# Kernel optimization log

Hardware: AMD Instinct MI355X
Metric: run time of the kernel (lower is better)

The kernel has to match this reference:

```python
import jax, jax.numpy as jnp
import numpy as np


def _skew_relative(QE):
    # QE: [B, H, N, 2N-1] -> [B, H, N, N] relative-position skew (Music-Transformer style)
    B, H, N, L = QE.shape  # L == 2N - 1
    x = jnp.pad(QE, ((0, 0), (0, 0), (0, 0), (0, 1))).reshape(B, H, N * (L + 1))
    x = jnp.pad(x, ((0, 0), (0, 0), (0, N - 1))).reshape(B, H, N + 1, 2 * N - 1)
    return x[:, :, :N, -N:]


def setup_inputs() -> dict:
    key = jax.random.key(0)
    ks = jax.random.split(key, 8)
    B, N, D, H, dh = 8, 1024, 512, 8, 64
    W_SCALE = 0.02
    return {
        "x": jax.random.normal(ks[0], (B, N, D), jnp.float32),
        "phase": jax.random.uniform(ks[1], (B, H, N, 1), jnp.float32),
        "E_rel": jax.random.normal(ks[2], (2 * N - 1, dh), jnp.float32) * 0.05,
        "W_q": jax.random.normal(ks[3], (H * dh, D), jnp.float32) * W_SCALE,
        "W_k": jax.random.normal(ks[4], (H * dh, D), jnp.float32) * W_SCALE,
        "W_v": jax.random.normal(ks[5], (H * dh, D), jnp.float32) * W_SCALE,
        "W_o": jax.random.normal(ks[6], (D, H * dh), jnp.float32) * W_SCALE,
        "b_o": jnp.zeros((D,), jnp.float32),
    }


def reference(x, phase, E_rel, W_q, W_k, W_v, W_o, b_o):
    B, N, _ = x.shape
    H = phase.shape[1]
    dh = W_q.shape[0] // H
    scale = 1.0 / (dh ** 0.5)

    def heads(W):  # [B,N,H*dh] -> [B,H,N,dh]
        return (x @ W.T).reshape(B, N, H, dh).transpose(0, 2, 1, 3)

    Q, K, V = heads(W_q), heads(W_k), heads(W_v)
    attn = jnp.einsum('bhnd,bhmd->bhnm', Q, K)
    attn = attn + _skew_relative(jnp.einsum('bhnd,ld->bhnl', Q, E_rel))
    attn = jax.nn.softmax(attn * scale, axis=-1)
    out = jnp.einsum('bhnm,bhmd->bhnd', attn, V) * phase  # phase-modulated AV
    out = out.transpose(0, 2, 1, 3).reshape(B, N, H * dh)
    return out @ W_o.T + b_o  # dropout is identity in eval mode
```

## Files before the change

### kernel.cpp

```cpp
#include <hip/hip_runtime.h>


typedef __bf16 bf16x8 __attribute__((ext_vector_type(8)));
typedef __bf16 bf16x4 __attribute__((ext_vector_type(4)));
typedef float  f32x4  __attribute__((ext_vector_type(4)));
typedef float  f32x16 __attribute__((ext_vector_type(16)));

#if __has_builtin(__builtin_amdgcn_exp2f)
#define EXP2(x) __builtin_amdgcn_exp2f(x)
#else
#define EXP2(x) exp2f(x)
#endif

#define GLOAD_LDS16(g, l)                                                      \
    __builtin_amdgcn_global_load_lds(                                          \
        (const __attribute__((address_space(1))) unsigned int*)(g),            \
        (__attribute__((address_space(3))) unsigned int*)(l), 16, 0, 0)


__global__ __launch_bounds__(256) void cvt_all(const float* __restrict__ x,
                                               const float* __restrict__ E,
                                               const float* __restrict__ wq,
                                               const float* __restrict__ wk,
                                               const float* __restrict__ wv,
                                               const float* __restrict__ wo,
                                               __bf16* __restrict__ xb,
                                               __bf16* __restrict__ Ef,
                                               __bf16* __restrict__ wqkv,
                                               __bf16* __restrict__ wob) {
    int i = blockIdx.x * 256 + threadIdx.x;
    if (i >= 1081328 ? i < 1343472 : i < 1048576) {
        const float* s; __bf16* d; int off;
        if      (i < 1048576) { s = x;  d = xb;            off = i; }
        else if (i < 1146864) { s = wq; d = wqkv;          off = i - 1081328; }
        else if (i < 1212400) { s = wk; d = wqkv + 262144; off = i - 1146864; }
        else if (i < 1277936) { s = wv; d = wqkv + 524288; off = i - 1212400; }
        else                  { s = wo; d = wob;           off = i - 1277936; }
        float4 v = *(const float4*)(s + (size_t)off * 4);
        bf16x4 o;
        o[0] = (__bf16)v.x; o[1] = (__bf16)v.y; o[2] = (__bf16)v.z; o[3] = (__bf16)v.w;
        *(bf16x4*)(d + (size_t)off * 4) = o;
    } else if (i >= 1048576 && i < 1081328) {
        int off = i - 1048576;
        float4 v = *(const float4*)(E + (size_t)off * 4);
        int e0i = off * 4;
        int l = e0i >> 6, d0 = e0i & 63;
        int t32 = l >> 5, cq = l & 31, ks = d0 >> 4, hf = (d0 >> 3) & 1, j = d0 & 7;
        bf16x4 o;
        o[0] = (__bf16)v.x; o[1] = (__bf16)v.y; o[2] = (__bf16)v.z; o[3] = (__bf16)v.w;
        *(bf16x4*)(Ef + ((size_t)((t32 * 4 + ks) * 64) + hf * 32 + cq) * 8 + j) = o;
    }
}

__global__ __launch_bounds__(256) void gemm_qkv(const __bf16* __restrict__ X,
                                                const __bf16* __restrict__ W,
                                                __bf16* __restrict__ Qb,
                                                __bf16* __restrict__ Kf,
                                                __bf16* __restrict__ Vf) {
    __shared__ __bf16 Xs[128][64];
    __shared__ __bf16 Ws[128][64];
    const int tid = threadIdx.x;
    const int wave = tid >> 6, lane = tid & 63;
    const int col = lane & 15, quad = lane >> 4;
    const int m_base = blockIdx.x * 128;
    const int j_base = blockIdx.y * 128;
    const bool qk = (j_base < 1024);
    const int wm = (wave & 1) * 64;
    const int wn = (wave >> 1) * 64;
    const f32x4 fz = {0.f, 0.f, 0.f, 0.f};
    f32x4 acc[4][4];
#pragma unroll
    for (int i = 0; i < 4; ++i)
#pragma unroll
        for (int j = 0; j < 4; ++j) acc[i][j] = fz;

    for (int k0 = 0; k0 < 512; k0 += 64) {
#pragma unroll
        for (int p = 0; p < 4; ++p) {
            int s = tid + p * 256;
            int row = s >> 3, cc = (s & 7) * 8;
            GLOAD_LDS16(X + (size_t)(m_base + row) * 512 + k0 + cc, &Xs[0][0] + (size_t)s * 8);
            GLOAD_LDS16(W + (size_t)(j_base + row) * 512 + k0 + cc, &Ws[0][0] + (size_t)s * 8);
        }
        __syncthreads();
#pragma unroll
        for (int kk = 0; kk < 64; kk += 32) {
            bf16x8 xa[4], wb[4];
#pragma unroll
            for (int i = 0; i < 4; ++i) xa[i] = *(const bf16x8*)(&Xs[wm + i * 16 + col][kk + quad * 8]);
#pragma unroll
            for (int j = 0; j < 4; ++j) wb[j] = *(const bf16x8*)(&Ws[wn + j * 16 + col][kk + quad * 8]);
            if (qk) {
#pragma unroll
                for (int i = 0; i < 4; ++i)
#pragma unroll
                    for (int j = 0; j < 4; ++j)
                        acc[i][j] = __builtin_amdgcn_mfma_f32_16x16x32_bf16(wb[i], xa[j], acc[i][j], 0, 0, 0);
            } else {
#pragma unroll
                for (int i = 0; i < 4; ++i)
#pragma unroll
                    for (int j = 0; j < 4; ++j)
                        acc[i][j] = __builtin_amdgcn_mfma_f32_16x16x32_bf16(xa[i], wb[j], acc[i][j], 0, 0, 0);
            }
        }
        __syncthreads();
    }
    if (qk) {
#pragma unroll
        for (int i = 0; i < 4; ++i) {
#pragma unroll
            for (int j = 0; j < 4; ++j) {
                int jabs = j_base + wn + i * 16 + quad * 4;
                int m = m_base + wm + j * 16 + col;
                int b_ = m >> 10, n = m & 1023;
                int rem = jabs & 511, h = rem >> 6, d = rem & 63;
                bf16x4 v;
                v[0] = (__bf16)acc[i][j][0]; v[1] = (__bf16)acc[i][j][1];
                v[2] = (__bf16)acc[i][j][2]; v[3] = (__bf16)acc[i][j][3];
                if (jabs < 512) {
                    *(bf16x4*)(Qb + (((size_t)b_ * 8 + h) * 1024 + n) * 64 + d) = v;
                } else {
                    int t32 = n >> 5, cq = n & 31, ks = d >> 4, hf = (d >> 3) & 1, jj = d & 7;
                    *(bf16x4*)(Kf + (size_t)(b_ * 8 + h) * 65536 +
                               ((size_t)((t32 * 4 + ks) * 64) + hf * 32 + cq) * 8 + jj) = v;
                }
            }
        }
    } else {
#pragma unroll
        for (int i = 0; i < 4; ++i) {
#pragma unroll
            for (int j = 0; j < 4; ++j) {
                int m = m_base + wm + i * 16 + quad * 4;
                int b_ = m >> 10, n = m & 1023;
                int jabs = j_base + wn + j * 16 + col;
                int rem = jabs & 511, h = rem >> 6, d = rem & 63;
                int t64 = n >> 6, ks = (n >> 4) & 3, hf = (n >> 3) & 1, jj = n & 7;
                int dhalf = d >> 5, cq = d & 31;
                bf16x4 v;
                v[0] = (__bf16)acc[i][j][0]; v[1] = (__bf16)acc[i][j][1];
                v[2] = (__bf16)acc[i][j][2]; v[3] = (__bf16)acc[i][j][3];
                *(bf16x4*)(Vf + (size_t)(b_ * 8 + h) * 65536 +
                           ((size_t)(((t64 * 4 + ks) * 2 + dhalf) * 64) + hf * 32 + cq) * 8 + jj) = v;
            }
        }
    }
}

__global__ __launch_bounds__(128) void flash_kernel(const __bf16* __restrict__ Qb,
                                                    const __bf16* __restrict__ Kf,
                                                    const __bf16* __restrict__ Vf,
                                                    const __bf16* __restrict__ Ef,
                                                    const float* __restrict__ phase,
                                                    __bf16* __restrict__ Ob) {
    const int bh = blockIdx.y;
    const int n0 = blockIdx.x * 64;
    const int w = threadIdx.x >> 6, lane = threadIdx.x & 63;
    const int colq = lane & 31, half = lane >> 5;
    const int nbase = n0 + w * 32;

    __shared__ __bf16 Pw[2][32][72];

    f32x16 z16;
#pragma unroll
    for (int i = 0; i < 16; ++i) z16[i] = 0.f;

    bf16x8 a_q[4];
#pragma unroll
    for (int ks = 0; ks < 4; ++ks)
        a_q[ks] = *(const bf16x8*)(Qb + ((size_t)bh * 1024 + nbase + colq) * 64 + ks * 16 + half * 8);

    f32x16 o0 = z16, o1 = z16;
    float rowsum[16];
#pragma unroll
    for (int i = 0; i < 16; ++i) rowsum[i] = 0.f;

    const __bf16* Kfb = Kf + (size_t)bh * 65536;
    const __bf16* Vfb = Vf + (size_t)bh * 65536;

#pragma unroll 1
    for (int m0 = 0; m0 < 1024; m0 += 64) {
        const int t32 = m0 >> 5;
        const int te = (m0 - nbase + 992) >> 5;
        f32x16 qe0 = z16, qe1 = z16, qe2 = z16, s0 = z16, s1 = z16;
#pragma unroll
        for (int ks = 0; ks < 4; ++ks) {
            bf16x8 e0 = *(const bf16x8*)(Ef + ((size_t)((te * 4 + ks) * 64) + lane) * 8);
            bf16x8 e1 = *(const bf16x8*)(Ef + ((size_t)(((te + 1) * 4 + ks) * 64) + lane) * 8);
            bf16x8 e2 = *(const bf16x8*)(Ef + ((size_t)(((te + 2) * 4 + ks) * 64) + lane) * 8);
            bf16x8 k0 = *(const bf16x8*)(Kfb + ((size_t)((t32 * 4 + ks) * 64) + lane) * 8);
            bf16x8 k1 = *(const bf16x8*)(Kfb + ((size_t)(((t32 + 1) * 4 + ks) * 64) + lane) * 8);
            qe0 = __builtin_amdgcn_mfma_f32_32x32x16_bf16(a_q[ks], e0, qe0, 0, 0, 0);
            qe1 = __builtin_amdgcn_mfma_f32_32x32x16_bf16(a_q[ks], e1, qe1, 0, 0, 0);
            qe2 = __builtin_amdgcn_mfma_f32_32x32x16_bf16(a_q[ks], e2, qe2, 0, 0, 0);
            s0  = __builtin_amdgcn_mfma_f32_32x32x16_bf16(a_q[ks], k0, s0, 0, 0, 0);
            s1  = __builtin_amdgcn_mfma_f32_32x32x16_bf16(a_q[ks], k1, s1, 0, 0, 0);
        }
#pragma unroll
        for (int r = 0; r < 16; ++r) {
            int row = (r & 3) + 8 * (r >> 2) + 4 * half;
            int t = colq + 31 - row;
            int src = (t & 31) | (half << 5);
            float sh0 = __shfl(qe0[r], src, 64);
            float sh1 = __shfl(qe1[r], src, 64);
            float sh2 = __shfl(qe2[r], src, 64);
            bool sel = (t >= 32);
            float rel0 = sel ? sh1 : sh0;
            float rel1 = sel ? sh2 : sh1;
            float p0 = EXP2((s0[r] + rel0) * 0.18033688f);
            float p1 = EXP2((s1[r] + rel1) * 0.18033688f);
            rowsum[r] += p0 + p1;
            Pw[w][row][colq]      = (__bf16)p0;
            Pw[w][row][32 + colq] = (__bf16)p1;
        }
        asm volatile("s_waitcnt lgkmcnt(0)" ::: "memory");
#pragma unroll
        for (int ks = 0; ks < 4; ++ks) {
            bf16x8 pa = *(const bf16x8*)(&Pw[w][colq][ks * 16 + half * 8]);
            bf16x8 v0 = *(const bf16x8*)(Vfb + ((size_t)((((m0 >> 6) * 4 + ks) * 2 + 0) * 64) + lane) * 8);
            bf16x8 v1 = *(const bf16x8*)(Vfb + ((size_t)((((m0 >> 6) * 4 + ks) * 2 + 1) * 64) + lane) * 8);
            o0 = __builtin_amdgcn_mfma_f32_32x32x16_bf16(pa, v0, o0, 0, 0, 0);
            o1 = __builtin_amdgcn_mfma_f32_32x32x16_bf16(pa, v1, o1, 0, 0, 0);
        }
        asm volatile("" ::: "memory");
    }

    const int b_ = bh >> 3, hh = bh & 7;
#pragma unroll
    for (int r = 0; r < 16; ++r) {
        float l = rowsum[r];
        l += __shfl_xor(l, 1, 32);
        l += __shfl_xor(l, 2, 32);
        l += __shfl_xor(l, 4, 32);
        l += __shfl_xor(l, 8, 32);
        l += __shfl_xor(l, 16, 32);
        int row = (r & 3) + 8 * (r >> 2) + 4 * half;
        float f = phase[(size_t)bh * 1024 + nbase + row] / l;
        Pw[w][row][colq]      = (__bf16)(o0[r] * f);
        Pw[w][row][32 + colq] = (__bf16)(o1[r] * f);
    }
    asm volatile("s_waitcnt lgkmcnt(0)" ::: "memory");
    {
        int row = lane >> 1, dseg = lane & 1;
        bf16x8 u0 = *(const bf16x8*)(&Pw[w][row][dseg * 32]);
        bf16x8 u1 = *(const bf16x8*)(&Pw[w][row][dseg * 32 + 8]);
        bf16x8 u2 = *(const bf16x8*)(&Pw[w][row][dseg * 32 + 16]);
        bf16x8 u3 = *(const bf16x8*)(&Pw[w][row][dseg * 32 + 24]);
        size_t obase = ((size_t)b_ * 1024 + nbase + row) * 512 + hh * 64 + dseg * 32;
        *(bf16x8*)(Ob + obase)      = u0;
        *(bf16x8*)(Ob + obase + 8)  = u1;
        *(bf16x8*)(Ob + obase + 16) = u2;
        *(bf16x8*)(Ob + obase + 24) = u3;
    }
}

__global__ __launch_bounds__(256) void gemm_out(const __bf16* __restrict__ X,
                                                const __bf16* __restrict__ W,
                                                const float* __restrict__ bo,
                                                float* __restrict__ out) {
    __shared__ __bf16 Xs[128][64];
    __shared__ __bf16 Ws[128][64];
    const int tid = threadIdx.x;
    const int wave = tid >> 6, lane = tid & 63;
    const int col = lane & 15, quad = lane >> 4;
    const int m_base = blockIdx.x * 128;
    const int j_base = blockIdx.y * 128;
    const int wm = (wave & 1) * 64;
    const int wn = (wave >> 1) * 64;
    const f32x4 fz = {0.f, 0.f, 0.f, 0.f};
    f32x4 acc[4][4];
#pragma unroll
    for (int i = 0; i < 4; ++i)
#pragma unroll
        for (int j = 0; j < 4; ++j) acc[i][j] = fz;

    for (int k0 = 0; k0 < 512; k0 += 64) {
#pragma unroll
        for (int p = 0; p < 4; ++p) {
            int s = tid + p * 256;
            int row = s >> 3, cc = (s & 7) * 8;
            GLOAD_LDS16(X + (size_t)(m_base + row) * 512 + k0 + cc, &Xs[0][0] + (size_t)s * 8);
            GLOAD_LDS16(W + (size_t)(j_base + row) * 512 + k0 + cc, &Ws[0][0] + (size_t)s * 8);
        }
        __syncthreads();
#pragma unroll
        for (int kk = 0; kk < 64; kk += 32) {
            bf16x8 xa[4], wb[4];
#pragma unroll
            for (int i = 0; i < 4; ++i) xa[i] = *(const bf16x8*)(&Xs[wm + i * 16 + col][kk + quad * 8]);
#pragma unroll
            for (int j = 0; j < 4; ++j) wb[j] = *(const bf16x8*)(&Ws[wn + j * 16 + col][kk + quad * 8]);
#pragma unroll
            for (int i = 0; i < 4; ++i)
#pragma unroll
                for (int j = 0; j < 4; ++j)
                    acc[i][j] = __builtin_amdgcn_mfma_f32_16x16x32_bf16(wb[i], xa[j], acc[i][j], 0, 0, 0);
        }
        __syncthreads();
    }
#pragma unroll
    for (int i = 0; i < 4; ++i) {
#pragma unroll
        for (int j = 0; j < 4; ++j) {
            int jabs = j_base + wn + i * 16 + quad * 4;
            int m = m_base + wm + j * 16 + col;
            f32x4 bv = *(const f32x4*)(bo + jabs);
            f32x4 o = acc[i][j] + bv;
            *(f32x4*)(out + (size_t)m * 512 + jabs) = o;
        }
    }
}

extern "C" void kernel_launch(void* const* d_in, const int* in_sizes, int n_in,
                              void* d_out, int out_size, void* d_ws, size_t ws_size,
                              hipStream_t stream) {
    (void)in_sizes; (void)n_in; (void)out_size; (void)ws_size;
    const float* x     = (const float*)d_in[0];
    const float* phase = (const float*)d_in[1];
    const float* E_rel = (const float*)d_in[2];
    const float* W_q   = (const float*)d_in[3];
    const float* W_k   = (const float*)d_in[4];
    const float* W_v   = (const float*)d_in[5];
    const float* W_o   = (const float*)d_in[6];
    const float* b_o   = (const float*)d_in[7];
    float* out = (float*)d_out;

    char* ws = (char*)d_ws;
    __bf16* xb   = (__bf16*)(ws);
    __bf16* wqkv = (__bf16*)(ws + 8388608);
    __bf16* wob  = (__bf16*)(ws + 9961472);
    __bf16* Ef   = (__bf16*)(ws + 10485760);
    __bf16* Qb   = (__bf16*)(ws + 10747904);
    __bf16* Kf   = (__bf16*)(ws + 19136512);
    __bf16* Vf   = (__bf16*)(ws + 27525120);
    __bf16* Ob   = (__bf16*)(ws + 35913728);

    cvt_all<<<dim3(5249), dim3(256), 0, stream>>>(x, E_rel, W_q, W_k, W_v, W_o,
                                                  xb, Ef, wqkv, wob);
    gemm_qkv<<<dim3(64, 12), dim3(256), 0, stream>>>(xb, wqkv, Qb, Kf, Vf);
    flash_kernel<<<dim3(16, 64), dim3(128), 0, stream>>>(Qb, Kf, Vf, Ef, phase, Ob);
    gemm_out<<<dim3(64, 4), dim3(256), 0, stream>>>(Ob, wob, b_o, out);
}
```

Before: 199.2 us.

## Split KV range across two waves per query tile and merge partials

Each block now handles one 32-row query tile, and its two waves each process half of the key/value positions in interleaved 64-wide chunks. The partial outputs and row sums are merged through shared memory before normalisation and the store. The grid becomes 1D with 2048 blocks and bh as the fast index, so blocks sharing K/V for a head run close together in time. This doubles block count and shortens each wave's serial loop, which raises parallelism. It costs a syncthreads, extra shared memory, and a serial merge epilogue. It also halves Q-tile reuse per block, so more blocks reload the same K/V data.

```diff
diff --git a/kernel.cpp b/kernel.cpp
--- a/kernel.cpp
+++ b/kernel.cpp
@@ -154,13 +154,15 @@
                                                     const __bf16* __restrict__ Ef,
                                                     const float* __restrict__ phase,
                                                     __bf16* __restrict__ Ob) {
-    const int bh = blockIdx.y;
-    const int n0 = blockIdx.x * 64;
+    const int bid = blockIdx.x;
+    const int bh = bid & 63;
+    const int nbase = (bid >> 6) * 32;
     const int w = threadIdx.x >> 6, lane = threadIdx.x & 63;
     const int colq = lane & 31, half = lane >> 5;
-    const int nbase = n0 + w * 32;
 
     __shared__ __bf16 Pw[2][32][72];
+    __shared__ float  Om[32][65];
+    __shared__ float  lsum[32];
 
     f32x16 z16;
 #pragma unroll
@@ -180,7 +182,8 @@
     const __bf16* Vfb = Vf + (size_t)bh * 65536;
 
 #pragma unroll 1
-    for (int m0 = 0; m0 < 1024; m0 += 64) {
+    for (int t = 0; t < 8; ++t) {
+        const int m0 = w * 64 + t * 128;
         const int t32 = m0 >> 5;
         const int te = (m0 - nbase + 992) >> 5;
         f32x16 qe0 = z16, qe1 = z16, qe2 = z16, s0 = z16, s1 = z16;
@@ -200,12 +203,12 @@
 #pragma unroll
         for (int r = 0; r < 16; ++r) {
             int row = (r & 3) + 8 * (r >> 2) + 4 * half;
-            int t = colq + 31 - row;
-            int src = (t & 31) | (half << 5);
+            int tt = colq + 31 - row;
+            int src = (tt & 31) | (half << 5);
             float sh0 = __shfl(qe0[r], src, 64);
             float sh1 = __shfl(qe1[r], src, 64);
             float sh2 = __shfl(qe2[r], src, 64);
-            bool sel = (t >= 32);
+            bool sel = (tt >= 32);
             float rel0 = sel ? sh1 : sh0;
             float rel1 = sel ? sh2 : sh1;
             float p0 = EXP2((s0[r] + rel0) * 0.18033688f);
@@ -226,7 +229,6 @@
         asm volatile("" ::: "memory");
     }
 
-    const int b_ = bh >> 3, hh = bh & 7;
 #pragma unroll
     for (int r = 0; r < 16; ++r) {
         float l = rowsum[r];
@@ -235,18 +237,34 @@
         l += __shfl_xor(l, 4, 32);
         l += __shfl_xor(l, 8, 32);
         l += __shfl_xor(l, 16, 32);
-        int row = (r & 3) + 8 * (r >> 2) + 4 * half;
-        float f = phase[(size_t)bh * 1024 + nbase + row] / l;
-        Pw[w][row][colq]      = (__bf16)(o0[r] * f);
-        Pw[w][row][32 + colq] = (__bf16)(o1[r] * f);
-    }
-    asm volatile("s_waitcnt lgkmcnt(0)" ::: "memory");
-    {
+        rowsum[r] = l;
+    }
+    if (w == 1) {
+#pragma unroll
+        for (int r = 0; r < 16; ++r) {
+            int row = (r & 3) + 8 * (r >> 2) + 4 * half;
+            Om[row][colq]      = o0[r];
+            Om[row][32 + colq] = o1[r];
+            if (colq == 0) lsum[row] = rowsum[r];
+        }
+    }
+    __syncthreads();
+    if (w == 0) {
+        const int b_ = bh >> 3, hh = bh & 7;
+#pragma unroll
+        for (int r = 0; r < 16; ++r) {
+            int row = (r & 3) + 8 * (r >> 2) + 4 * half;
+            float l = rowsum[r] + lsum[row];
+            float f = phase[(size_t)bh * 1024 + nbase + row] / l;
+            Pw[0][row][colq]      = (__bf16)((o0[r] + Om[row][colq]) * f);
+            Pw[0][row][32 + colq] = (__bf16)((o1[r] + Om[row][32 + colq]) * f);
+        }
+        asm volatile("s_waitcnt lgkmcnt(0)" ::: "memory");
         int row = lane >> 1, dseg = lane & 1;
-        bf16x8 u0 = *(const bf16x8*)(&Pw[w][row][dseg * 32]);
-        bf16x8 u1 = *(const bf16x8*)(&Pw[w][row][dseg * 32 + 8]);
-        bf16x8 u2 = *(const bf16x8*)(&Pw[w][row][dseg * 32 + 16]);
-        bf16x8 u3 = *(const bf16x8*)(&Pw[w][row][dseg * 32 + 24]);
+        bf16x8 u0 = *(const bf16x8*)(&Pw[0][row][dseg * 32]);
+        bf16x8 u1 = *(const bf16x8*)(&Pw[0][row][dseg * 32 + 8]);
+        bf16x8 u2 = *(const bf16x8*)(&Pw[0][row][dseg * 32 + 16]);
+        bf16x8 u3 = *(const bf16x8*)(&Pw[0][row][dseg * 32 + 24]);
         size_t obase = ((size_t)b_ * 1024 + nbase + row) * 512 + hh * 64 + dseg * 32;
         *(bf16x8*)(Ob + obase)      = u0;
         *(bf16x8*)(Ob + obase + 8)  = u1;
@@ -339,6 +357,6 @@
     cvt_all<<<dim3(5249), dim3(256), 0, stream>>>(x, E_rel, W_q, W_k, W_v, W_o,
                                                   xb, Ef, wqkv, wob);
     gemm_qkv<<<dim3(64, 12), dim3(256), 0, stream>>>(xb, wqkv, Qb, Kf, Vf);
-    flash_kernel<<<dim3(16, 64), dim3(128), 0, stream>>>(Qb, Kf, Vf, Ef, phase, Ob);
+    flash_kernel<<<dim3(2048), dim3(128), 0, stream>>>(Qb, Kf, Vf, Ef, phase, Ob);
     gemm_out<<<dim3(64, 4), dim3(256), 0, stream>>>(Ob, wob, b_o, out);
 }
```

Result: slower. 258.1 us (+29.6%).
